# Optimization experiments

Measured on AMD Instinct MI355X. Metric: run time of the kernel, lower is better.

The kernel has to match this reference:

```python
import jax, jax.numpy as jnp
import numpy as np
import math

B, N, D_MODEL, D_QK, D_V = 8, 2048, 512, 64, 64
NEG_INF = float('-inf')

def setup_inputs() -> dict:
    key = jax.random.key(0)
    k1, k2, k3, k4, k5 = jax.random.split(key, 5)
    mask = jax.random.randint(k1, (B, N, N), 0, 2).astype(bool)
    x_key_value = jax.random.normal(k2, (B, N, D_MODEL), dtype=jnp.float32)
    wk = jax.random.normal(k3, (D_MODEL, D_QK), dtype=jnp.float32) * 0.02
    wq = jax.random.normal(k4, (D_MODEL, D_QK), dtype=jnp.float32) * 0.02
    wv = jax.random.normal(k5, (D_MODEL, D_V), dtype=jnp.float32) * 0.02
    return {"mask": mask, "x_key_value": x_key_value, "wk": wk, "wq": wq, "wv": wv}

def reference(mask, x_key_value, wk, wq, wv):
    # self-attention: x_query defaults to x_key_value
    div = math.sqrt(wk.shape[1])
    k = x_key_value @ wk          # [n, j, d_qk]
    q = x_key_value @ wq          # [n, i, d_qk]
    v = x_key_value @ wv          # [n, j, d_v]
    mat = jnp.einsum('nik,njk->nij', q, k) / div
    mat = jnp.where(mask, mat, NEG_INF)
    portion = jax.nn.softmax(mat, axis=2)
    return jnp.einsum('nij,njk->nik', portion, v)
```

## Files before the change

### kernel.cpp

```cpp
#include <hip/hip_runtime.h>
#include <hip/hip_bf16.h>

typedef __attribute__((ext_vector_type(8))) short bf16x8;
typedef __attribute__((ext_vector_type(4))) float f32x4;
typedef __hip_bfloat16 bf16;

#define BATCH 8
#define SEQ   2048
#define DMODEL 512
#define DHEAD 64
#define ROWS (BATCH * SEQ)

static __device__ inline short f2bf(float f) {
    union { __hip_bfloat16 h; short s; } u;
    u.h = __float2bfloat16(f);
    return u.s;
}


__global__ __launch_bounds__(256) void transpose_w_kernel(
    const float* __restrict__ wq, const float* __restrict__ wk,
    const float* __restrict__ wv, bf16* __restrict__ wt)
{
    int idx = blockIdx.x * 256 + threadIdx.x;
    int s = idx >> 15;
    int r = idx & 32767;
    int n = r >> 9;
    int k = r & 511;
    const float* w = (s == 0) ? wq : ((s == 1) ? wk : wv);
    union { __hip_bfloat16 h; bf16 b; } u;
    u.h = __float2bfloat16(w[k * DHEAD + n]);
    wt[idx] = u.b;
}

__global__ __launch_bounds__(512) void proj_kernel(
    const float* __restrict__ x, const bf16* __restrict__ wt,
    bf16* __restrict__ Q, bf16* __restrict__ K, bf16* __restrict__ Vt)
{
    const int r0 = blockIdx.x * 64;

    __shared__ __align__(16) bf16 Xs[64][72];
    __shared__ __align__(16) bf16 Ws[192][72];

    const int tid = threadIdx.x;
    const int lane = tid & 63;
    const int wid = tid >> 6;
    const int w4 = wid & 3;
    const int whalf = wid >> 2;
    const int l15 = lane & 15;
    const int quad = lane >> 4;

    f32x4 acc[6] = {};

    const int xrow = tid >> 3;
    const int xseg = tid & 7;

    for (int k0 = 0; k0 < DMODEL; k0 += 64) {
        const float* xp = x + (size_t)(r0 + xrow) * DMODEL + k0 + xseg * 8;
        float4 xa = *(const float4*)(xp);
        float4 xb = *(const float4*)(xp + 4);
        bf16x8 xv;
        xv[0] = f2bf(xa.x); xv[1] = f2bf(xa.y); xv[2] = f2bf(xa.z); xv[3] = f2bf(xa.w);
        xv[4] = f2bf(xb.x); xv[5] = f2bf(xb.y); xv[6] = f2bf(xb.z); xv[7] = f2bf(xb.w);
        *(bf16x8*)(&Xs[xrow][xseg * 8]) = xv;

#pragma unroll
        for (int s = 0; s < 3; ++s) {
            int sid = tid + s * 512;
            int wr = sid >> 3;
            int wc = (sid & 7) * 8;
            *(uint4*)(&Ws[wr][wc]) = *(const uint4*)(wt + (size_t)wr * DMODEL + k0 + wc);
        }
        __syncthreads();

        bf16x8 a0 = *(const bf16x8*)(&Xs[16 * w4 + l15][quad * 8]);
        bf16x8 a1 = *(const bf16x8*)(&Xs[16 * w4 + l15][32 + quad * 8]);
#pragma unroll
        for (int c = 0; c < 6; ++c) {
            int cg = whalf * 6 + c;
            bf16x8 b0 = *(const bf16x8*)(&Ws[16 * cg + l15][quad * 8]);
            bf16x8 b1 = *(const bf16x8*)(&Ws[16 * cg + l15][32 + quad * 8]);
            acc[c] = __builtin_amdgcn_mfma_f32_16x16x32_bf16(a0, b0, acc[c], 0, 0, 0);
            acc[c] = __builtin_amdgcn_mfma_f32_16x16x32_bf16(a1, b1, acc[c], 0, 0, 0);
        }
        __syncthreads();
    }

#pragma unroll
    for (int c = 0; c < 6; ++c) {
        int ng = 16 * (whalf * 6 + c) + l15;
        int sel = ng >> 6;
        int col = ng & 63;
#pragma unroll
        for (int r = 0; r < 4; ++r) {
            int row = r0 + 16 * w4 + quad * 4 + r;
            union { __hip_bfloat16 h; bf16 b; } u;
            u.h = __float2bfloat16(acc[c][r]);
            if (sel == 0)      Q[(size_t)row * DHEAD + col] = u.b;
            else if (sel == 1) K[(size_t)row * DHEAD + col] = u.b;
            else {
                int bb = row >> 11, j = row & (SEQ - 1);
                Vt[((size_t)bb * DHEAD + col) * SEQ + j] = u.b;
            }
        }
    }
}

__global__ __launch_bounds__(128) void flash_kernel(
    const bf16* __restrict__ Q, const bf16* __restrict__ K,
    const bf16* __restrict__ Vt, const int* __restrict__ mask,
    float* __restrict__ out)
{
    const int b = blockIdx.y;
    const int q0 = blockIdx.x * 32;
    const int tid = threadIdx.x;
    const int lane = tid & 63;
    const int wid = tid >> 6;
    const int l15 = lane & 15;
    const int quad = lane >> 4;

    __shared__ __align__(16) bf16 Ps[32][72];

    const bf16* qp = Q + ((size_t)(b * SEQ + q0 + 16 * wid + l15)) * DHEAD + quad * 8;
    bf16x8 aQ0 = *(const bf16x8*)(qp);
    bf16x8 aQ1 = *(const bf16x8*)(qp + 32);

    f32x4 oacc[4] = {};
    float m_i[4], l_i[4];
#pragma unroll
    for (int r = 0; r < 4; ++r) { m_i[r] = -1e30f; l_i[r] = 0.f; }

    const size_t mrow0 = ((size_t)b * SEQ + (size_t)(q0 + 16 * wid + quad * 4)) * SEQ;

    for (int jt = 0; jt < SEQ / 64; ++jt) {
        const int j0 = jt * 64;

        f32x4 sacc[4] = {};
#pragma unroll
        for (int c = 0; c < 4; ++c) {
            const bf16* kp = K + ((size_t)(b * SEQ + j0 + 16 * c + l15)) * DHEAD + quad * 8;
            bf16x8 b0 = *(const bf16x8*)(kp);
            bf16x8 b1 = *(const bf16x8*)(kp + 32);
            sacc[c] = __builtin_amdgcn_mfma_f32_16x16x32_bf16(aQ0, b0, sacc[c], 0, 0, 0);
            sacc[c] = __builtin_amdgcn_mfma_f32_16x16x32_bf16(aQ1, b1, sacc[c], 0, 0, 0);
        }

        float sv[4][4];
#pragma unroll
        for (int c = 0; c < 4; ++c) {
#pragma unroll
            for (int r = 0; r < 4; ++r) {
                int mv = mask[mrow0 + (size_t)r * SEQ + (j0 + 16 * c + l15)];
                sv[c][r] = mv ? sacc[c][r] * 0.125f : -1e30f;
            }
        }

#pragma unroll
        for (int r = 0; r < 4; ++r) {
            float rm = fmaxf(fmaxf(sv[0][r], sv[1][r]), fmaxf(sv[2][r], sv[3][r]));
            rm = fmaxf(rm, __shfl_xor(rm, 1));
            rm = fmaxf(rm, __shfl_xor(rm, 2));
            rm = fmaxf(rm, __shfl_xor(rm, 4));
            rm = fmaxf(rm, __shfl_xor(rm, 8));
            float mn = fmaxf(m_i[r], rm);
            float alpha = exp2f((m_i[r] - mn) * 1.44269504f);
            m_i[r] = mn;
            float rs = 0.f;
#pragma unroll
            for (int c = 0; c < 4; ++c) {
                float pv = exp2f((sv[c][r] - mn) * 1.44269504f);
                sv[c][r] = pv;
                rs += pv;
            }
            rs += __shfl_xor(rs, 1);
            rs += __shfl_xor(rs, 2);
            rs += __shfl_xor(rs, 4);
            rs += __shfl_xor(rs, 8);
            l_i[r] = l_i[r] * alpha + rs;
#pragma unroll
            for (int c = 0; c < 4; ++c) oacc[c][r] *= alpha;
        }

#pragma unroll
        for (int c = 0; c < 4; ++c)
#pragma unroll
            for (int r = 0; r < 4; ++r) {
                union { __hip_bfloat16 h; bf16 b; } u;
                u.h = __float2bfloat16(sv[c][r]);
                Ps[16 * wid + quad * 4 + r][16 * c + l15] = u.b;
            }
        __syncthreads();

        bf16x8 aP0 = *(const bf16x8*)(&Ps[16 * wid + l15][quad * 8]);
        bf16x8 aP1 = *(const bf16x8*)(&Ps[16 * wid + l15][32 + quad * 8]);
#pragma unroll
        for (int c = 0; c < 4; ++c) {
            const bf16* vp = Vt + ((size_t)b * DHEAD + 16 * c + l15) * SEQ + j0 + quad * 8;
            bf16x8 v0 = *(const bf16x8*)(vp);
            bf16x8 v1 = *(const bf16x8*)(vp + 32);
            oacc[c] = __builtin_amdgcn_mfma_f32_16x16x32_bf16(aP0, v0, oacc[c], 0, 0, 0);
            oacc[c] = __builtin_amdgcn_mfma_f32_16x16x32_bf16(aP1, v1, oacc[c], 0, 0, 0);
        }
        __syncthreads();
    }

#pragma unroll
    for (int r = 0; r < 4; ++r) {
        float inv = 1.0f / l_i[r];
#pragma unroll
        for (int c = 0; c < 4; ++c) {
            int qr = q0 + 16 * wid + quad * 4 + r;
            out[((size_t)b * SEQ + qr) * DHEAD + 16 * c + l15] = oacc[c][r] * inv;
        }
    }
}

extern "C" void kernel_launch(void* const* d_in, const int* in_sizes, int n_in,
                              void* d_out, int out_size, void* d_ws, size_t ws_size,
                              hipStream_t stream)
{
    const int*   mask = (const int*)d_in[0];
    const float* x    = (const float*)d_in[1];
    const float* wk   = (const float*)d_in[2];
    const float* wq   = (const float*)d_in[3];
    const float* wv   = (const float*)d_in[4];
    float* out = (float*)d_out;

    bf16* Qb = (bf16*)d_ws;
    bf16* Kb = Qb + (size_t)ROWS * DHEAD;
    bf16* Vt = Kb + (size_t)ROWS * DHEAD;
    bf16* Wt = Vt + (size_t)BATCH * DHEAD * SEQ;

    transpose_w_kernel<<<dim3(3 * 64 * DMODEL / 256), 256, 0, stream>>>(wq, wk, wv, Wt);
    proj_kernel<<<dim3(ROWS / 64), 512, 0, stream>>>(x, Wt, Qb, Kb, Vt);
    flash_kernel<<<dim3(SEQ / 32, BATCH), 128, 0, stream>>>(Qb, Kb, Vt, mask, out);
}
```

Before: 305.6 us.

## Split KV range across waves in flash kernel and restructure projection/transposes

The flash kernel now gives each block 16 query rows and splits the key range into four quarters, one per wave. Each wave keeps its own online-softmax state, and the partial outputs are merged through shared memory at the end. This removes the per-tile block barriers and doubles the number of blocks, which should raise parallelism for the mask-bandwidth-bound attention. The projection kernel now reads X and W straight from global memory into registers with no LDS staging, at the cost of redundant global reads. The weight transpose is tiled through shared memory.

```diff
diff --git a/kernel.cpp b/kernel.cpp
--- a/kernel.cpp
+++ b/kernel.cpp
@@ -10,6 +10,7 @@
 #define DMODEL 512
 #define DHEAD 64
 #define ROWS (BATCH * SEQ)
+#define LOG2E 1.44269504f
 
 static __device__ inline short f2bf(float f) {
     union { __hip_bfloat16 h; short s; } u;
@@ -17,85 +18,86 @@
     return u.s;
 }
 
-
 __global__ __launch_bounds__(256) void transpose_w_kernel(
     const float* __restrict__ wq, const float* __restrict__ wk,
     const float* __restrict__ wv, bf16* __restrict__ wt)
 {
-    int idx = blockIdx.x * 256 + threadIdx.x;
-    int s = idx >> 15;
-    int r = idx & 32767;
-    int n = r >> 9;
-    int k = r & 511;
+    const int s  = blockIdx.x / 8;
+    const int kt = blockIdx.x % 8;
     const float* w = (s == 0) ? wq : ((s == 1) ? wk : wv);
-    union { __hip_bfloat16 h; bf16 b; } u;
-    u.h = __float2bfloat16(w[k * DHEAD + n]);
-    wt[idx] = u.b;
+
+    __shared__ float Ts[64][68];
+
+    const int tid = threadIdx.x;
+    int nr = tid >> 4;
+    int n4 = (tid & 15) * 4;
+#pragma unroll
+    for (int p = 0; p < 4; ++p) {
+        int k = 16 * p + nr;
+        float4 v = *(const float4*)(w + (size_t)(kt * 64 + k) * DHEAD + n4);
+        Ts[k][n4] = v.x; Ts[k][n4 + 1] = v.y; Ts[k][n4 + 2] = v.z; Ts[k][n4 + 3] = v.w;
+    }
+    __syncthreads();
+#pragma unroll
+    for (int p = 0; p < 2; ++p) {
+        int cc = tid + p * 256;
+        int n = cc >> 3;
+        int kk = (cc & 7) * 8;
+        bf16x8 o;
+#pragma unroll
+        for (int e = 0; e < 8; ++e) o[e] = f2bf(Ts[kk + e][n]);
+        *(bf16x8*)(wt + (size_t)(s * 64 + n) * DMODEL + kt * 64 + kk) = o;
+    }
 }
 
 __global__ __launch_bounds__(512) void proj_kernel(
     const float* __restrict__ x, const bf16* __restrict__ wt,
     bf16* __restrict__ Q, bf16* __restrict__ K, bf16* __restrict__ Vt)
 {
-    const int r0 = blockIdx.x * 64;
-
-    __shared__ __align__(16) bf16 Xs[64][72];
-    __shared__ __align__(16) bf16 Ws[192][72];
-
+    const int r0 = blockIdx.x * 32;
     const int tid = threadIdx.x;
     const int lane = tid & 63;
     const int wid = tid >> 6;
-    const int w4 = wid & 3;
-    const int whalf = wid >> 2;
+    const int strip = wid & 1;
+    const int cq = wid >> 1;
     const int l15 = lane & 15;
     const int quad = lane >> 4;
 
-    f32x4 acc[6] = {};
-
-    const int xrow = tid >> 3;
-    const int xseg = tid & 7;
+    f32x4 acc[3] = {};
+
+    const float* xp = x + (size_t)(r0 + 16 * strip + l15) * DMODEL;
 
     for (int k0 = 0; k0 < DMODEL; k0 += 64) {
-        const float* xp = x + (size_t)(r0 + xrow) * DMODEL + k0 + xseg * 8;
-        float4 xa = *(const float4*)(xp);
-        float4 xb = *(const float4*)(xp + 4);
-        bf16x8 xv;
-        xv[0] = f2bf(xa.x); xv[1] = f2bf(xa.y); xv[2] = f2bf(xa.z); xv[3] = f2bf(xa.w);
-        xv[4] = f2bf(xb.x); xv[5] = f2bf(xb.y); xv[6] = f2bf(xb.z); xv[7] = f2bf(xb.w);
-        *(bf16x8*)(&Xs[xrow][xseg * 8]) = xv;
-
-#pragma unroll
-        for (int s = 0; s < 3; ++s) {
-            int sid = tid + s * 512;
-            int wr = sid >> 3;
-            int wc = (sid & 7) * 8;
-            *(uint4*)(&Ws[wr][wc]) = *(const uint4*)(wt + (size_t)wr * DMODEL + k0 + wc);
-        }
-        __syncthreads();
-
-        bf16x8 a0 = *(const bf16x8*)(&Xs[16 * w4 + l15][quad * 8]);
-        bf16x8 a1 = *(const bf16x8*)(&Xs[16 * w4 + l15][32 + quad * 8]);
-#pragma unroll
-        for (int c = 0; c < 6; ++c) {
-            int cg = whalf * 6 + c;
-            bf16x8 b0 = *(const bf16x8*)(&Ws[16 * cg + l15][quad * 8]);
-            bf16x8 b1 = *(const bf16x8*)(&Ws[16 * cg + l15][32 + quad * 8]);
-            acc[c] = __builtin_amdgcn_mfma_f32_16x16x32_bf16(a0, b0, acc[c], 0, 0, 0);
-            acc[c] = __builtin_amdgcn_mfma_f32_16x16x32_bf16(a1, b1, acc[c], 0, 0, 0);
-        }
-        __syncthreads();
-    }
-
-#pragma unroll
-    for (int c = 0; c < 6; ++c) {
-        int ng = 16 * (whalf * 6 + c) + l15;
+        float4 xa = *(const float4*)(xp + k0 + quad * 8);
+        float4 xb = *(const float4*)(xp + k0 + quad * 8 + 4);
+        float4 xc = *(const float4*)(xp + k0 + 32 + quad * 8);
+        float4 xd = *(const float4*)(xp + k0 + 32 + quad * 8 + 4);
+        bf16x8 a0, a1;
+        a0[0] = f2bf(xa.x); a0[1] = f2bf(xa.y); a0[2] = f2bf(xa.z); a0[3] = f2bf(xa.w);
+        a0[4] = f2bf(xb.x); a0[5] = f2bf(xb.y); a0[6] = f2bf(xb.z); a0[7] = f2bf(xb.w);
+        a1[0] = f2bf(xc.x); a1[1] = f2bf(xc.y); a1[2] = f2bf(xc.z); a1[3] = f2bf(xc.w);
+        a1[4] = f2bf(xd.x); a1[5] = f2bf(xd.y); a1[6] = f2bf(xd.z); a1[7] = f2bf(xd.w);
+#pragma unroll
+        for (int g = 0; g < 3; ++g) {
+            int n = 16 * (3 * cq + g) + l15;
+            const bf16* wp = wt + (size_t)n * DMODEL + k0 + quad * 8;
+            bf16x8 b0 = *(const bf16x8*)(wp);
+            bf16x8 b1 = *(const bf16x8*)(wp + 32);
+            acc[g] = __builtin_amdgcn_mfma_f32_16x16x32_bf16(a0, b0, acc[g], 0, 0, 0);
+            acc[g] = __builtin_amdgcn_mfma_f32_16x16x32_bf16(a1, b1, acc[g], 0, 0, 0);
+        }
+    }
+
+#pragma unroll
+    for (int g = 0; g < 3; ++g) {
+        int ng = 16 * (3 * cq + g) + l15;
         int sel = ng >> 6;
         int col = ng & 63;
 #pragma unroll
         for (int r = 0; r < 4; ++r) {
-            int row = r0 + 16 * w4 + quad * 4 + r;
+            int row = r0 + 16 * strip + quad * 4 + r;
             union { __hip_bfloat16 h; bf16 b; } u;
-            u.h = __float2bfloat16(acc[c][r]);
+            u.h = __float2bfloat16(acc[g][r]);
             if (sel == 0)      Q[(size_t)row * DHEAD + col] = u.b;
             else if (sel == 1) K[(size_t)row * DHEAD + col] = u.b;
             else {
@@ -106,22 +108,25 @@
     }
 }
 
-__global__ __launch_bounds__(128) void flash_kernel(
+__global__ __launch_bounds__(256) void flash_kernel(
     const bf16* __restrict__ Q, const bf16* __restrict__ K,
     const bf16* __restrict__ Vt, const int* __restrict__ mask,
     float* __restrict__ out)
 {
     const int b = blockIdx.y;
-    const int q0 = blockIdx.x * 32;
+    const int q0 = blockIdx.x * 16;
     const int tid = threadIdx.x;
     const int lane = tid & 63;
     const int wid = tid >> 6;
     const int l15 = lane & 15;
     const int quad = lane >> 4;
 
-    __shared__ __align__(16) bf16 Ps[32][72];
-
-    const bf16* qp = Q + ((size_t)(b * SEQ + q0 + 16 * wid + l15)) * DHEAD + quad * 8;
+    __shared__ __align__(16) bf16 Ps[4][16][72];
+    __shared__ float Om[4][16][64];
+    __shared__ float Mw[4][16];
+    __shared__ float Lw[4][16];
+
+    const bf16* qp = Q + ((size_t)(b * SEQ + q0 + l15)) * DHEAD + quad * 8;
     bf16x8 aQ0 = *(const bf16x8*)(qp);
     bf16x8 aQ1 = *(const bf16x8*)(qp + 32);
 
@@ -130,10 +135,11 @@
 #pragma unroll
     for (int r = 0; r < 4; ++r) { m_i[r] = -1e30f; l_i[r] = 0.f; }
 
-    const size_t mrow0 = ((size_t)b * SEQ + (size_t)(q0 + 16 * wid + quad * 4)) * SEQ;
-
-    for (int jt = 0; jt < SEQ / 64; ++jt) {
-        const int j0 = jt * 64;
+    const int* mp = mask + ((size_t)(b * SEQ + q0 + quad * 4)) * SEQ;
+    const int jbase = wid * (SEQ / 4);
+
+    for (int jt = 0; jt < SEQ / 4; jt += 64) {
+        const int j0 = jbase + jt;
 
         f32x4 sacc[4] = {};
 #pragma unroll
@@ -145,31 +151,30 @@
             sacc[c] = __builtin_amdgcn_mfma_f32_16x16x32_bf16(aQ1, b1, sacc[c], 0, 0, 0);
         }
 
-        float sv[4][4];
 #pragma unroll
         for (int c = 0; c < 4; ++c) {
 #pragma unroll
             for (int r = 0; r < 4; ++r) {
-                int mv = mask[mrow0 + (size_t)r * SEQ + (j0 + 16 * c + l15)];
-                sv[c][r] = mv ? sacc[c][r] * 0.125f : -1e30f;
+                int mv = mp[(size_t)r * SEQ + (j0 + 16 * c + l15)];
+                sacc[c][r] = mv ? sacc[c][r] * 0.125f : -1e30f;
             }
         }
 
 #pragma unroll
         for (int r = 0; r < 4; ++r) {
-            float rm = fmaxf(fmaxf(sv[0][r], sv[1][r]), fmaxf(sv[2][r], sv[3][r]));
+            float rm = fmaxf(fmaxf(sacc[0][r], sacc[1][r]), fmaxf(sacc[2][r], sacc[3][r]));
             rm = fmaxf(rm, __shfl_xor(rm, 1));
             rm = fmaxf(rm, __shfl_xor(rm, 2));
             rm = fmaxf(rm, __shfl_xor(rm, 4));
             rm = fmaxf(rm, __shfl_xor(rm, 8));
             float mn = fmaxf(m_i[r], rm);
-            float alpha = exp2f((m_i[r] - mn) * 1.44269504f);
+            float alpha = exp2f((m_i[r] - mn) * LOG2E);
             m_i[r] = mn;
             float rs = 0.f;
 #pragma unroll
             for (int c = 0; c < 4; ++c) {
-                float pv = exp2f((sv[c][r] - mn) * 1.44269504f);
-                sv[c][r] = pv;
+                float pv = exp2f((sacc[c][r] - mn) * LOG2E);
+                sacc[c][r] = pv;
                 rs += pv;
             }
             rs += __shfl_xor(rs, 1);
@@ -186,13 +191,12 @@
 #pragma unroll
             for (int r = 0; r < 4; ++r) {
                 union { __hip_bfloat16 h; bf16 b; } u;
-                u.h = __float2bfloat16(sv[c][r]);
-                Ps[16 * wid + quad * 4 + r][16 * c + l15] = u.b;
-            }
-        __syncthreads();
-
-        bf16x8 aP0 = *(const bf16x8*)(&Ps[16 * wid + l15][quad * 8]);
-        bf16x8 aP1 = *(const bf16x8*)(&Ps[16 * wid + l15][32 + quad * 8]);
+                u.h = __float2bfloat16(sacc[c][r]);
+                Ps[wid][quad * 4 + r][16 * c + l15] = u.b;
+            }
+
+        bf16x8 aP0 = *(const bf16x8*)(&Ps[wid][l15][quad * 8]);
+        bf16x8 aP1 = *(const bf16x8*)(&Ps[wid][l15][32 + quad * 8]);
 #pragma unroll
         for (int c = 0; c < 4; ++c) {
             const bf16* vp = Vt + ((size_t)b * DHEAD + 16 * c + l15) * SEQ + j0 + quad * 8;
@@ -201,17 +205,40 @@
             oacc[c] = __builtin_amdgcn_mfma_f32_16x16x32_bf16(aP0, v0, oacc[c], 0, 0, 0);
             oacc[c] = __builtin_amdgcn_mfma_f32_16x16x32_bf16(aP1, v1, oacc[c], 0, 0, 0);
         }
-        __syncthreads();
-    }
-
-#pragma unroll
-    for (int r = 0; r < 4; ++r) {
-        float inv = 1.0f / l_i[r];
-#pragma unroll
-        for (int c = 0; c < 4; ++c) {
-            int qr = q0 + 16 * wid + quad * 4 + r;
-            out[((size_t)b * SEQ + qr) * DHEAD + 16 * c + l15] = oacc[c][r] * inv;
-        }
+    }
+
+#pragma unroll
+    for (int c = 0; c < 4; ++c)
+#pragma unroll
+        for (int r = 0; r < 4; ++r)
+            Om[wid][quad * 4 + r][16 * c + l15] = oacc[c][r];
+    if (l15 == 0) {
+#pragma unroll
+        for (int r = 0; r < 4; ++r) {
+            Mw[wid][quad * 4 + r] = m_i[r];
+            Lw[wid][quad * 4 + r] = l_i[r];
+        }
+    }
+    __syncthreads();
+
+    {
+        int row = tid >> 4;
+        int c0 = (tid & 15) * 4;
+        float M = fmaxf(fmaxf(Mw[0][row], Mw[1][row]), fmaxf(Mw[2][row], Mw[3][row]));
+        float sc0 = exp2f((Mw[0][row] - M) * LOG2E);
+        float sc1 = exp2f((Mw[1][row] - M) * LOG2E);
+        float sc2 = exp2f((Mw[2][row] - M) * LOG2E);
+        float sc3 = exp2f((Mw[3][row] - M) * LOG2E);
+        float L = Lw[0][row] * sc0 + Lw[1][row] * sc1 + Lw[2][row] * sc2 + Lw[3][row] * sc3;
+        float invL = 1.0f / L;
+        float4 o;
+        float* op = (float*)&o;
+#pragma unroll
+        for (int e = 0; e < 4; ++e) {
+            op[e] = (Om[0][row][c0 + e] * sc0 + Om[1][row][c0 + e] * sc1 +
+                     Om[2][row][c0 + e] * sc2 + Om[3][row][c0 + e] * sc3) * invL;
+        }
+        *(float4*)(out + ((size_t)(b * SEQ + q0 + row)) * DHEAD + c0) = o;
     }
 }
 
@@ -231,7 +258,7 @@
     bf16* Vt = Kb + (size_t)ROWS * DHEAD;
     bf16* Wt = Vt + (size_t)BATCH * DHEAD * SEQ;
 
-    transpose_w_kernel<<<dim3(3 * 64 * DMODEL / 256), 256, 0, stream>>>(wq, wk, wv, Wt);
-    proj_kernel<<<dim3(ROWS / 64), 512, 0, stream>>>(x, Wt, Qb, Kb, Vt);
-    flash_kernel<<<dim3(SEQ / 32, BATCH), 128, 0, stream>>>(Qb, Kb, Vt, mask, out);
-}
+    transpose_w_kernel<<<dim3(24), 256, 0, stream>>>(wq, wk, wv, Wt);
+    proj_kernel<<<dim3(ROWS / 32), 512, 0, stream>>>(x, Wt, Qb, Kb, Vt);
+    flash_kernel<<<dim3(SEQ / 16, BATCH), 256, 0, stream>>>(Qb, Kb, Vt, mask, out);
+}
```

Measured after the change: 299.1 us. 1.02x faster.
